# Optimization experiments

Hardware: AMD Instinct MI355X
Metric: run time of the kernel (lower is better)

Reference implementation:

```python
import jax, jax.numpy as jnp
import numpy as np

HEADS = 8
DIM_HEAD = 64
INNER = HEADS * DIM_HEAD  # 512
EPS = 1e-6


def layer_norm(x, gamma, beta):
    mu = jnp.mean(x, axis=-1, keepdims=True)
    var = jnp.var(x, axis=-1, keepdims=True)
    return (x - mu) * jax.lax.rsqrt(var + EPS) * gamma + beta


def setup_inputs() -> dict:
    key = jax.random.key(0)
    ks = jax.random.split(key, 8)
    b, n = 2, 2048
    s = lambda d: 1.0 / np.sqrt(d)
    return {
        "x": jax.random.normal(ks[0], (b, n, INNER), dtype=jnp.float32),
        # weights stored input-major: y = x @ W
        "w_qkv": jax.random.normal(ks[1], (INNER, 3 * INNER), dtype=jnp.float32) * s(INNER),
        "w_out": jax.random.normal(ks[2], (INNER, INNER), dtype=jnp.float32) * s(INNER),
        "b_out": jax.random.normal(ks[3], (INNER,), dtype=jnp.float32) * 0.01,
        "w_ff1": jax.random.normal(ks[4], (INNER, 4 * INNER), dtype=jnp.float32) * s(INNER),
        "w_ff2": jax.random.normal(ks[5], (4 * INNER, INNER), dtype=jnp.float32) * s(4 * INNER),
        "g1": jnp.ones((INNER,), dtype=jnp.float32),
        "be1": jnp.zeros((INNER,), dtype=jnp.float32),
        "g2": jnp.ones((INNER,), dtype=jnp.float32),
        "be2": jnp.zeros((INNER,), dtype=jnp.float32),
    }


def reference(x, w_qkv, w_out, b_out, w_ff1, w_ff2, g1, be1, g2, be2):
    b, n, _ = x.shape
    scale = DIM_HEAD ** (-0.5)
    qkv = x @ w_qkv  # [b, n, 3*inner]
    qkv = qkv.reshape(b, n, 3, HEADS, DIM_HEAD)
    q = qkv[:, :, 0].transpose(0, 2, 1, 3)  # [b, h, n, d]
    k = qkv[:, :, 1].transpose(0, 2, 1, 3)
    v = qkv[:, :, 2].transpose(0, 2, 1, 3)
    dots = jnp.einsum('bhqd,bhkd->bhqk', q, k) * scale
    attn = jax.nn.softmax(dots, axis=-1)
    out = jnp.einsum('bhqk,bhkd->bhqd', attn, v)
    out = out.transpose(0, 2, 1, 3).reshape(b, n, INNER)
    out = out @ w_out + b_out
    attn_res = layer_norm(x + out, g1, be1)
    # NOTE: no activation between the two FFN linears (faithful to source)
    ff = (attn_res @ w_ff1) @ w_ff2
    return layer_norm(attn_res + ff, g2, be2)
```

## Files before the change

### kernel.cpp

```cpp
#include <hip/hip_runtime.h>
#include <hip/hip_bf16.h>
#include <cstdint>
#include <cstddef>
#include <math.h>

#define HEADS 8
#define DHEAD 64
#define INNER 512
#define BATCH 2
#define SEQ   2048
#define MROWS (BATCH*SEQ)
#define LN_EPS 1e-6f
#define KSPLIT 2
#define KCHUNK (SEQ/KSPLIT)

typedef unsigned short u16;
typedef __attribute__((ext_vector_type(8))) short short8;
typedef __attribute__((ext_vector_type(4))) float f32x4;

#define MFMA16(a,b,c) __builtin_amdgcn_mfma_f32_16x16x32_bf16((a),(b),(c),0,0,0)

__device__ __forceinline__ u16 f2bf(float f) {
    __hip_bfloat16 h = __float2bfloat16(f);
    return *reinterpret_cast<u16*>(&h);
}
__device__ __forceinline__ void gl_lds16(const void* g, void* l) {
    __builtin_amdgcn_global_load_lds(
        (const __attribute__((address_space(1))) void*)g,
        (__attribute__((address_space(3))) void*)l, 16, 0, 0);
}

__global__ void f32_to_bf16_kernel(const float* __restrict__ in,
                                   u16* __restrict__ out, int n4) {
    int i = (blockIdx.x * 256 + threadIdx.x);
    if (i < n4) {
        float4 v = reinterpret_cast<const float4*>(in)[i];
        ushort4 o;
        o.x = f2bf(v.x); o.y = f2bf(v.y); o.z = f2bf(v.z); o.w = f2bf(v.w);
        reinterpret_cast<ushort4*>(out)[i] = o;
    }
}

__global__ void transpose_to_bf16_kernel(const float* __restrict__ B,
                                         u16* __restrict__ Bt, int K, int N) {
    __shared__ float T[32][33];
    const int tid = threadIdx.x;
    const int n0 = blockIdx.x * 32, k0 = blockIdx.y * 32;
    const int r = tid >> 3, c = (tid & 7) * 4;
    float4 v = *reinterpret_cast<const float4*>(&B[(size_t)(k0 + r) * N + n0 + c]);
    T[c + 0][r] = v.x; T[c + 1][r] = v.y; T[c + 2][r] = v.z; T[c + 3][r] = v.w;
    __syncthreads();
    ushort4 o;
    o.x = f2bf(T[r][c + 0]); o.y = f2bf(T[r][c + 1]);
    o.z = f2bf(T[r][c + 2]); o.w = f2bf(T[r][c + 3]);
    *reinterpret_cast<ushort4*>(&Bt[(size_t)(n0 + r) * K + k0 + c]) = o;
}

template<int BN, bool HAS_BIAS, bool OUT_F32, bool OUT_BF16>
__global__ __launch_bounds__(256) void gemm_bt(const u16* __restrict__ A,
                                               const u16* __restrict__ Bt,
                                               const float* __restrict__ bias,
                                               float* __restrict__ C,
                                               u16* __restrict__ Cb,
                                               int M, int N, int K) {
    constexpr int WN = BN / 2;
    constexpr int NT = WN / 16;
    __shared__ u16 As[128 * 32];
    __shared__ u16 Bs[BN * 32];
    const int tid = threadIdx.x;
    const int wave = tid >> 6, lane = tid & 63;
    const int l15 = lane & 15, quad = lane >> 4;
    const int wm = (wave >> 1) * 64, wn = (wave & 1) * WN;
    const int row0 = blockIdx.y * 128, col0 = blockIdx.x * BN;

    f32x4 acc[4][NT];
    #pragma unroll
    for (int mi = 0; mi < 4; ++mi)
        #pragma unroll
        for (int ni = 0; ni < NT; ++ni)
            #pragma unroll
            for (int e = 0; e < 4; ++e) acc[mi][ni][e] = 0.f;

    for (int k0 = 0; k0 < K; k0 += 32) {
        #pragma unroll
        for (int idx0 = 0; idx0 < 512 + BN * 4; idx0 += 256) {
            int idx = idx0 + tid;
            if (idx < 512) {
                int r = idx >> 2, ic = (idx & 3) * 8;
                gl_lds16(A + (size_t)(row0 + r) * K + k0 + ic, &As[idx * 8]);
            } else {
                int ib = idx - 512;
                int r = ib >> 2, ic = (ib & 3) * 8;
                gl_lds16(Bt + (size_t)(col0 + r) * K + k0 + ic, &Bs[ib * 8]);
            }
        }
        __syncthreads();

        short8 af[4], bf[NT];
        #pragma unroll
        for (int mi = 0; mi < 4; ++mi)
            af[mi] = *reinterpret_cast<const short8*>(&As[(wm + mi * 16 + l15) * 32 + quad * 8]);
        #pragma unroll
        for (int ni = 0; ni < NT; ++ni)
            bf[ni] = *reinterpret_cast<const short8*>(&Bs[(wn + ni * 16 + l15) * 32 + quad * 8]);
        #pragma unroll
        for (int mi = 0; mi < 4; ++mi)
            #pragma unroll
            for (int ni = 0; ni < NT; ++ni)
                acc[mi][ni] = MFMA16(af[mi], bf[ni], acc[mi][ni]);
        __syncthreads();
    }

    #pragma unroll
    for (int mi = 0; mi < 4; ++mi)
        #pragma unroll
        for (int ni = 0; ni < NT; ++ni)
            #pragma unroll
            for (int r = 0; r < 4; ++r) {
                int rr = row0 + wm + mi * 16 + quad * 4 + r;
                int cc = col0 + wn + ni * 16 + l15;
                float v = acc[mi][ni][r];
                if (HAS_BIAS) v += bias[cc];
                if (OUT_F32)  C[(size_t)rr * N + cc] = v;
                if (OUT_BF16) Cb[(size_t)rr * N + cc] = f2bf(v);
            }
}

__global__ __launch_bounds__(256) void attn_kernel(const u16* __restrict__ qkv,
                                                   float* __restrict__ Opart,
                                                   float* __restrict__ lpart) {
    __shared__ u16 QP[64][72];
    __shared__ u16 Ks[64][72];
    __shared__ u16 VT[64][72];

    const int tid = threadIdx.x;
    const int wave = tid >> 6, lane = tid & 63;
    const int l15 = lane & 15, quad = lane >> 4;
    const int qt = blockIdx.x, bh = blockIdx.y, ks = blockIdx.z;
    const int b = bh >> 3, h = bh & 7;
    const int w16 = wave * 16;

    const u16* qbase = qkv + (size_t)(b * SEQ + qt * 64) * 1536 + h * 64;

    #pragma unroll
    for (int j = 0; j < 2; ++j) {
        int c = tid + j * 256;
        int r = c >> 3, ch = c & 7;
        *reinterpret_cast<uint4*>(&QP[r][ch * 8]) =
            *reinterpret_cast<const uint4*>(qbase + (size_t)r * 1536 + ch * 8);
    }
    __syncthreads();

    short8 qf[2];
    #pragma unroll
    for (int ksk = 0; ksk < 2; ++ksk)
        qf[ksk] = *reinterpret_cast<const short8*>(&QP[w16 + l15][ksk * 32 + quad * 8]);

    f32x4 oacc[4];
    float lsum[4];
    #pragma unroll
    for (int di = 0; di < 4; ++di)
        #pragma unroll
        for (int e = 0; e < 4; ++e) oacc[di][e] = 0.f;
    #pragma unroll
    for (int r = 0; r < 4; ++r) lsum[r] = 0.f;

    const float scale = 0.125f;

    for (int kt = 0; kt < KCHUNK / 64; ++kt) {
        const u16* kvbase = qkv +
            (size_t)(b * SEQ + ks * KCHUNK + kt * 64) * 1536 + h * 64;
        #pragma unroll
        for (int j = 0; j < 2; ++j) {
            int c = tid + j * 256;
            int r = c >> 3, ch = c & 7;
            *reinterpret_cast<uint4*>(&Ks[r][ch * 8]) =
                *reinterpret_cast<const uint4*>(kvbase + 512 + (size_t)r * 1536 + ch * 8);
        }
        {
            int kj = tid & 63, d0 = (tid >> 6) * 16;
            const u16* vp = kvbase + 1024 + (size_t)kj * 1536 + d0;
            u16 tmp[16];
            *reinterpret_cast<uint4*>(tmp)     = *reinterpret_cast<const uint4*>(vp);
            *reinterpret_cast<uint4*>(tmp + 8) = *reinterpret_cast<const uint4*>(vp + 8);
            #pragma unroll
            for (int i = 0; i < 16; ++i) VT[d0 + i][kj] = tmp[i];
        }
        __syncthreads();

        f32x4 sacc[4];
        #pragma unroll
        for (int ni = 0; ni < 4; ++ni)
            #pragma unroll
            for (int e = 0; e < 4; ++e) sacc[ni][e] = 0.f;
        #pragma unroll
        for (int ksk = 0; ksk < 2; ++ksk) {
            short8 kf[4];
            #pragma unroll
            for (int ni = 0; ni < 4; ++ni)
                kf[ni] = *reinterpret_cast<const short8*>(
                    &Ks[ni * 16 + l15][ksk * 32 + quad * 8]);
            #pragma unroll
            for (int ni = 0; ni < 4; ++ni)
                sacc[ni] = MFMA16(qf[ksk], kf[ni], sacc[ni]);
        }

        #pragma unroll
        for (int ni = 0; ni < 4; ++ni)
            #pragma unroll
            for (int r = 0; r < 4; ++r) {
                float p = __expf(sacc[ni][r] * scale);
                lsum[r] += p;
                QP[w16 + quad * 4 + r][ni * 16 + l15] = f2bf(p);
            }

        #pragma unroll
        for (int ksk = 0; ksk < 2; ++ksk) {
            short8 pf = *reinterpret_cast<const short8*>(
                &QP[w16 + l15][ksk * 32 + quad * 8]);
            #pragma unroll
            for (int di = 0; di < 4; ++di) {
                short8 vf = *reinterpret_cast<const short8*>(
                    &VT[di * 16 + l15][ksk * 32 + quad * 8]);
                oacc[di] = MFMA16(pf, vf, oacc[di]);
            }
        }
        __syncthreads();
    }

    #pragma unroll
    for (int r = 0; r < 4; ++r) {
        float v = lsum[r];
        v += __shfl_xor(v, 1); v += __shfl_xor(v, 2);
        v += __shfl_xor(v, 4); v += __shfl_xor(v, 8);
        lsum[r] = v;
    }

    const size_t pbase = ((size_t)(ks * 16 + bh) * SEQ + qt * 64);
    #pragma unroll
    for (int di = 0; di < 4; ++di)
        #pragma unroll
        for (int r = 0; r < 4; ++r)
            Opart[(pbase + w16 + quad * 4 + r) * 64 + di * 16 + l15] = oacc[di][r];
    if (l15 == 0)
        #pragma unroll
        for (int r = 0; r < 4; ++r)
            lpart[pbase + w16 + quad * 4 + r] = lsum[r];
}

__global__ void attn_combine_kernel(const float* __restrict__ Opart,
                                    const float* __restrict__ lpart,
                                    u16* __restrict__ attn_b) {
    int i = blockIdx.x * 256 + threadIdx.x;
    int e = i * 4;
    int row = e >> 9;
    int c = e & 511;
    int h = c >> 6, d = c & 63;
    int b = row >> 11, srow = row & 2047;
    int bh = b * 8 + h;

    size_t i0 = ((size_t)bh * SEQ + srow) * 64 + d;
    size_t i1 = ((size_t)(16 + bh) * SEQ + srow) * 64 + d;
    float4 o0 = *reinterpret_cast<const float4*>(&Opart[i0]);
    float4 o1 = *reinterpret_cast<const float4*>(&Opart[i1]);
    float l = lpart[(size_t)bh * SEQ + srow] + lpart[(size_t)(16 + bh) * SEQ + srow];
    float li = 1.f / l;
    ushort4 o;
    o.x = f2bf((o0.x + o1.x) * li);
    o.y = f2bf((o0.y + o1.y) * li);
    o.z = f2bf((o0.z + o1.z) * li);
    o.w = f2bf((o0.w + o1.w) * li);
    *reinterpret_cast<ushort4*>(&attn_b[(size_t)row * INNER + c]) = o;
}

__global__ void ln_kernel(const float* __restrict__ a,
                          const float* __restrict__ bsrc,
                          const float* __restrict__ g,
                          const float* __restrict__ be,
                          float* __restrict__ out32,
                          u16* __restrict__ out16) {
    __shared__ float red[256];
    const int row = blockIdx.x, tid = threadIdx.x;
    const size_t off = (size_t)row * INNER;
    const int c0 = tid, c1 = tid + 256;

    float v0 = a[off + c0] + bsrc[off + c0];
    float v1 = a[off + c1] + bsrc[off + c1];

    red[tid] = v0 + v1;
    __syncthreads();
    for (int s = 128; s > 0; s >>= 1) {
        if (tid < s) red[tid] += red[tid + s];
        __syncthreads();
    }
    float mu = red[0] * (1.f / INNER);
    __syncthreads();

    float d0 = v0 - mu, d1 = v1 - mu;
    red[tid] = d0 * d0 + d1 * d1;
    __syncthreads();
    for (int s = 128; s > 0; s >>= 1) {
        if (tid < s) red[tid] += red[tid + s];
        __syncthreads();
    }
    float rstd = rsqrtf(red[0] * (1.f / INNER) + LN_EPS);

    float y0 = d0 * rstd * g[c0] + be[c0];
    float y1 = d1 * rstd * g[c1] + be[c1];
    if (out32) { out32[off + c0] = y0; out32[off + c1] = y1; }
    if (out16) { out16[off + c0] = f2bf(y0); out16[off + c1] = f2bf(y1); }
}

extern "C" void kernel_launch(void* const* d_in, const int* in_sizes, int n_in,
                              void* d_out, int out_size, void* d_ws, size_t ws_size,
                              hipStream_t stream) {
    const float* x     = (const float*)d_in[0];
    const float* w_qkv = (const float*)d_in[1];
    const float* w_out = (const float*)d_in[2];
    const float* b_out = (const float*)d_in[3];
    const float* w_ff1 = (const float*)d_in[4];
    const float* w_ff2 = (const float*)d_in[5];
    const float* g1    = (const float*)d_in[6];
    const float* be1   = (const float*)d_in[7];
    const float* g2    = (const float*)d_in[8];
    const float* be2   = (const float*)d_in[9];
    float* out = (float*)d_out;

    char* W = (char*)d_ws;
    u16*   w_outT     = (u16*)  (W + 0);
    u16*   w_ff1T     = (u16*)  (W + 524288);
    u16*   w_ff2T     = (u16*)  (W + 2621440);
    u16*   qkv_b      = (u16*)  (W + 4718592);
    float* proj       = (float*)(W + 4718592);
    float* ff2        = (float*)(W + 4718592);
    u16*   attn_res_b = (u16*)  (W + 13107200);
    u16*   x_b        = (u16*)  (W + 17301504);
    u16*   w_qkvT     = (u16*)  (W + 21495808);
    float* Opart      = (float*)(W + 17301504);
    u16*   ff1_b      = (u16*)  (W + 17301504);
    float* lpart      = (float*)(W + 34078720);
    u16*   attn_b     = (u16*)  (W + 34340864);
    float* attn_res   = (float*)(W + 38535168);

    f32_to_bf16_kernel<<<(MROWS * INNER / 4 + 255) / 256, 256, 0, stream>>>(
        x, x_b, MROWS * INNER / 4);
    transpose_to_bf16_kernel<<<dim3(1536 / 32, 512 / 32),  256, 0, stream>>>(w_qkv, w_qkvT, 512, 1536);
    transpose_to_bf16_kernel<<<dim3(512 / 32,  512 / 32),  256, 0, stream>>>(w_out, w_outT, 512, 512);
    transpose_to_bf16_kernel<<<dim3(2048 / 32, 512 / 32),  256, 0, stream>>>(w_ff1, w_ff1T, 512, 2048);
    transpose_to_bf16_kernel<<<dim3(512 / 32,  2048 / 32), 256, 0, stream>>>(w_ff2, w_ff2T, 2048, 512);

    gemm_bt<128, false, false, true><<<dim3(1536 / 128, MROWS / 128), 256, 0, stream>>>(
        x_b, w_qkvT, nullptr, nullptr, qkv_b, MROWS, 1536, INNER);

    attn_kernel<<<dim3(SEQ / 64, BATCH * HEADS, KSPLIT), 256, 0, stream>>>(
        qkv_b, Opart, lpart);

    attn_combine_kernel<<<(MROWS * INNER / 4) / 256, 256, 0, stream>>>(
        Opart, lpart, attn_b);

    gemm_bt<64, true, true, false><<<dim3(INNER / 64, MROWS / 128), 256, 0, stream>>>(
        attn_b, w_outT, b_out, proj, nullptr, MROWS, INNER, INNER);

    ln_kernel<<<MROWS, 256, 0, stream>>>(x, proj, g1, be1, attn_res, attn_res_b);

    gemm_bt<128, false, false, true><<<dim3(2048 / 128, MROWS / 128), 256, 0, stream>>>(
        attn_res_b, w_ff1T, nullptr, nullptr, ff1_b, MROWS, 2048, INNER);

    gemm_bt<64, false, true, false><<<dim3(INNER / 64, MROWS / 128), 256, 0, stream>>>(
        ff1_b, w_ff2T, nullptr, ff2, nullptr, MROWS, INNER, 2048);

    ln_kernel<<<MROWS, 256, 0, stream>>>(attn_res, ff2, g2, be2, out, nullptr);
}
```

Measured before the change: 242.2 us.

## Write Q/K and transposed V from QKV GEMM, prefetch attention tiles, split-K FF2

```diff
diff --git a/kernel.cpp b/kernel.cpp
--- a/kernel.cpp
+++ b/kernel.cpp
@@ -20,6 +20,9 @@
 
 #define MFMA16(a,b,c) __builtin_amdgcn_mfma_f32_16x16x32_bf16((a),(b),(c),0,0,0)
 
+__device__ __forceinline__ float bf2f(u16 u) {
+    union { float f; uint32_t i; } x; x.i = ((uint32_t)u) << 16; return x.f;
+}
 __device__ __forceinline__ u16 f2bf(float f) {
     __hip_bfloat16 h = __float2bfloat16(f);
     return *reinterpret_cast<u16*>(&h);
@@ -56,12 +59,13 @@
     *reinterpret_cast<ushort4*>(&Bt[(size_t)(n0 + r) * K + k0 + c]) = o;
 }
 
-template<int BN, bool HAS_BIAS, bool OUT_F32, bool OUT_BF16>
+template<int BN, int EPI>
 __global__ __launch_bounds__(256) void gemm_bt(const u16* __restrict__ A,
                                                const u16* __restrict__ Bt,
                                                const float* __restrict__ bias,
                                                float* __restrict__ C,
                                                u16* __restrict__ Cb,
+                                               u16* __restrict__ Vt,
                                                int M, int N, int K) {
     constexpr int WN = BN / 2;
     constexpr int NT = WN / 16;
@@ -73,6 +77,12 @@
     const int wm = (wave >> 1) * 64, wn = (wave & 1) * WN;
     const int row0 = blockIdx.y * 128, col0 = blockIdx.x * BN;
 
+    int kbase = 0, kend = K;
+    if (EPI == 3) {
+        int chunk = K / gridDim.z;
+        kbase = blockIdx.z * chunk; kend = kbase + chunk;
+    }
+
     f32x4 acc[4][NT];
     #pragma unroll
     for (int mi = 0; mi < 4; ++mi)
@@ -81,7 +91,7 @@
             #pragma unroll
             for (int e = 0; e < 4; ++e) acc[mi][ni][e] = 0.f;
 
-    for (int k0 = 0; k0 < K; k0 += 32) {
+    for (int k0 = kbase; k0 < kend; k0 += 32) {
         #pragma unroll
         for (int idx0 = 0; idx0 < 512 + BN * 4; idx0 += 256) {
             int idx = idx0 + tid;
@@ -114,19 +124,44 @@
     #pragma unroll
     for (int mi = 0; mi < 4; ++mi)
         #pragma unroll
-        for (int ni = 0; ni < NT; ++ni)
-            #pragma unroll
-            for (int r = 0; r < 4; ++r) {
-                int rr = row0 + wm + mi * 16 + quad * 4 + r;
-                int cc = col0 + wn + ni * 16 + l15;
-                float v = acc[mi][ni][r];
-                if (HAS_BIAS) v += bias[cc];
-                if (OUT_F32)  C[(size_t)rr * N + cc] = v;
-                if (OUT_BF16) Cb[(size_t)rr * N + cc] = f2bf(v);
+        for (int ni = 0; ni < NT; ++ni) {
+            const int cc = col0 + wn + ni * 16 + l15;
+            const int rr0 = row0 + wm + mi * 16 + quad * 4;
+            if (EPI == 0) {
+                #pragma unroll
+                for (int r = 0; r < 4; ++r)
+                    Cb[(size_t)(rr0 + r) * N + cc] = f2bf(acc[mi][ni][r]);
+            } else if (EPI == 1) {
+                #pragma unroll
+                for (int r = 0; r < 4; ++r)
+                    C[(size_t)(rr0 + r) * N + cc] = acc[mi][ni][r] + bias[cc];
+            } else if (EPI == 3) {
+                float* Cz = C + (size_t)blockIdx.z * M * N;
+                #pragma unroll
+                for (int r = 0; r < 4; ++r)
+                    Cz[(size_t)(rr0 + r) * N + cc] = acc[mi][ni][r];
+            } else {
+                if (cc < 1024) {
+                    size_t base = (cc < 512) ? (size_t)cc
+                                             : ((size_t)MROWS * 512 + cc - 512);
+                    #pragma unroll
+                    for (int r = 0; r < 4; ++r)
+                        Cb[base + (size_t)(rr0 + r) * 512] = f2bf(acc[mi][ni][r]);
+                } else {
+                    int hh = (cc - 1024) >> 6, dd = (cc - 1024) & 63;
+                    int bb = rr0 >> 11, srow = rr0 & 2047;
+                    ushort4 o;
+                    o.x = f2bf(acc[mi][ni][0]); o.y = f2bf(acc[mi][ni][1]);
+                    o.z = f2bf(acc[mi][ni][2]); o.w = f2bf(acc[mi][ni][3]);
+                    *reinterpret_cast<ushort4*>(
+                        &Vt[(((size_t)(bb * 8 + hh) * 64 + dd) << 11) + srow]) = o;
+                }
             }
-}
-
-__global__ __launch_bounds__(256) void attn_kernel(const u16* __restrict__ qkv,
+        }
+}
+
+__global__ __launch_bounds__(256) void attn_kernel(const u16* __restrict__ qk_b,
+                                                   const u16* __restrict__ vT_b,
                                                    float* __restrict__ Opart,
                                                    float* __restrict__ lpart) {
     __shared__ u16 QP[64][72];
@@ -139,22 +174,21 @@
     const int qt = blockIdx.x, bh = blockIdx.y, ks = blockIdx.z;
     const int b = bh >> 3, h = bh & 7;
     const int w16 = wave * 16;
-
-    const u16* qbase = qkv + (size_t)(b * SEQ + qt * 64) * 1536 + h * 64;
-
-    #pragma unroll
-    for (int j = 0; j < 2; ++j) {
-        int c = tid + j * 256;
-        int r = c >> 3, ch = c & 7;
-        *reinterpret_cast<uint4*>(&QP[r][ch * 8]) =
-            *reinterpret_cast<const uint4*>(qbase + (size_t)r * 1536 + ch * 8);
+    const int r0 = tid >> 3, r1 = r0 + 32;
+    const int ch = (tid & 7) * 8;
+
+    {
+        const u16* qb = qk_b + (size_t)(b * SEQ + qt * 64) * 512 + h * 64;
+        *reinterpret_cast<uint4*>(&QP[r0][ch]) =
+            *reinterpret_cast<const uint4*>(&qb[(size_t)r0 * 512 + ch]);
+        *reinterpret_cast<uint4*>(&QP[r1][ch]) =
+            *reinterpret_cast<const uint4*>(&qb[(size_t)r1 * 512 + ch]);
     }
     __syncthreads();
 
     short8 qf[2];
-    #pragma unroll
-    for (int ksk = 0; ksk < 2; ++ksk)
-        qf[ksk] = *reinterpret_cast<const short8*>(&QP[w16 + l15][ksk * 32 + quad * 8]);
+    qf[0] = *reinterpret_cast<const short8*>(&QP[w16 + l15][quad * 8]);
+    qf[1] = *reinterpret_cast<const short8*>(&QP[w16 + l15][32 + quad * 8]);
 
     f32x4 oacc[4];
     float lsum[4];
@@ -165,28 +199,32 @@
     #pragma unroll
     for (int r = 0; r < 4; ++r) lsum[r] = 0.f;
 
-    const float scale = 0.125f;
+    const u16* kb = qk_b + (size_t)MROWS * 512
+                  + (size_t)(b * SEQ + ks * KCHUNK) * 512 + h * 64;
+    const u16* vb = vT_b + (size_t)bh * 64 * 2048 + ks * KCHUNK;
+
+    uint4 kr0 = *reinterpret_cast<const uint4*>(&kb[(size_t)r0 * 512 + ch]);
+    uint4 kr1 = *reinterpret_cast<const uint4*>(&kb[(size_t)r1 * 512 + ch]);
+    uint4 vr0 = *reinterpret_cast<const uint4*>(&vb[(size_t)r0 * 2048 + ch]);
+    uint4 vr1 = *reinterpret_cast<const uint4*>(&vb[(size_t)r1 * 2048 + ch]);
+
+    const float CEXP = 0.18033688011110918f;
 
     for (int kt = 0; kt < KCHUNK / 64; ++kt) {
-        const u16* kvbase = qkv +
-            (size_t)(b * SEQ + ks * KCHUNK + kt * 64) * 1536 + h * 64;
-        #pragma unroll
-        for (int j = 0; j < 2; ++j) {
-            int c = tid + j * 256;
-            int r = c >> 3, ch = c & 7;
-            *reinterpret_cast<uint4*>(&Ks[r][ch * 8]) =
-                *reinterpret_cast<const uint4*>(kvbase + 512 + (size_t)r * 1536 + ch * 8);
+        *reinterpret_cast<uint4*>(&Ks[r0][ch]) = kr0;
+        *reinterpret_cast<uint4*>(&Ks[r1][ch]) = kr1;
+        *reinterpret_cast<uint4*>(&VT[r0][ch]) = vr0;
+        *reinterpret_cast<uint4*>(&VT[r1][ch]) = vr1;
+        __syncthreads();
+
+        if (kt + 1 < KCHUNK / 64) {
+            const u16* kb2 = kb + (size_t)(kt + 1) * 64 * 512;
+            const u16* vb2 = vb + (kt + 1) * 64;
+            kr0 = *reinterpret_cast<const uint4*>(&kb2[(size_t)r0 * 512 + ch]);
+            kr1 = *reinterpret_cast<const uint4*>(&kb2[(size_t)r1 * 512 + ch]);
+            vr0 = *reinterpret_cast<const uint4*>(&vb2[(size_t)r0 * 2048 + ch]);
+            vr1 = *reinterpret_cast<const uint4*>(&vb2[(size_t)r1 * 2048 + ch]);
         }
-        {
-            int kj = tid & 63, d0 = (tid >> 6) * 16;
-            const u16* vp = kvbase + 1024 + (size_t)kj * 1536 + d0;
-            u16 tmp[16];
-            *reinterpret_cast<uint4*>(tmp)     = *reinterpret_cast<const uint4*>(vp);
-            *reinterpret_cast<uint4*>(tmp + 8) = *reinterpret_cast<const uint4*>(vp + 8);
-            #pragma unroll
-            for (int i = 0; i < 16; ++i) VT[d0 + i][kj] = tmp[i];
-        }
-        __syncthreads();
 
         f32x4 sacc[4];
         #pragma unroll
@@ -209,7 +247,7 @@
         for (int ni = 0; ni < 4; ++ni)
             #pragma unroll
             for (int r = 0; r < 4; ++r) {
-                float p = __expf(sacc[ni][r] * scale);
+                float p = exp2f(sacc[ni][r] * CEXP);
                 lsum[r] += p;
                 QP[w16 + quad * 4 + r][ni * 16 + l15] = f2bf(p);
             }
@@ -273,8 +311,10 @@
     *reinterpret_cast<ushort4*>(&attn_b[(size_t)row * INNER + c]) = o;
 }
 
-__global__ void ln_kernel(const float* __restrict__ a,
-                          const float* __restrict__ bsrc,
+template<bool A16, bool TWO>
+__global__ void ln_kernel(const void* __restrict__ a_,
+                          const float* __restrict__ s0,
+                          const float* __restrict__ s1,
                           const float* __restrict__ g,
                           const float* __restrict__ be,
                           float* __restrict__ out32,
@@ -284,8 +324,17 @@
     const size_t off = (size_t)row * INNER;
     const int c0 = tid, c1 = tid + 256;
 
-    float v0 = a[off + c0] + bsrc[off + c0];
-    float v1 = a[off + c1] + bsrc[off + c1];
+    float a0, a1;
+    if (A16) {
+        const u16* a = (const u16*)a_;
+        a0 = bf2f(a[off + c0]); a1 = bf2f(a[off + c1]);
+    } else {
+        const float* a = (const float*)a_;
+        a0 = a[off + c0]; a1 = a[off + c1];
+    }
+    float v0 = a0 + s0[off + c0];
+    float v1 = a1 + s0[off + c1];
+    if (TWO) { v0 += s1[off + c0]; v1 += s1[off + c1]; }
 
     red[tid] = v0 + v1;
     __syncthreads();
@@ -330,17 +379,17 @@
     u16*   w_outT     = (u16*)  (W + 0);
     u16*   w_ff1T     = (u16*)  (W + 524288);
     u16*   w_ff2T     = (u16*)  (W + 2621440);
-    u16*   qkv_b      = (u16*)  (W + 4718592);
-    float* proj       = (float*)(W + 4718592);
-    float* ff2        = (float*)(W + 4718592);
-    u16*   attn_res_b = (u16*)  (W + 13107200);
+    u16*   qk_b       = (u16*)  (W + 4718592);
+    u16*   attn_b     = (u16*)  (W + 4718592);
+    u16*   attn_res_b = (u16*)  (W + 4718592);
+    float* proj       = (float*)(W + 8912896);
+    u16*   ff1_b      = (u16*)  (W + 8912896);
+    u16*   vT_b       = (u16*)  (W + 13107200);
     u16*   x_b        = (u16*)  (W + 17301504);
     u16*   w_qkvT     = (u16*)  (W + 21495808);
     float* Opart      = (float*)(W + 17301504);
-    u16*   ff1_b      = (u16*)  (W + 17301504);
     float* lpart      = (float*)(W + 34078720);
-    u16*   attn_b     = (u16*)  (W + 34340864);
-    float* attn_res   = (float*)(W + 38535168);
+    float* ff2p       = (float*)(W + 25690112);
 
     f32_to_bf16_kernel<<<(MROWS * INNER / 4 + 255) / 256, 256, 0, stream>>>(
         x, x_b, MROWS * INNER / 4);
@@ -349,25 +398,27 @@
     transpose_to_bf16_kernel<<<dim3(2048 / 32, 512 / 32),  256, 0, stream>>>(w_ff1, w_ff1T, 512, 2048);
     transpose_to_bf16_kernel<<<dim3(512 / 32,  2048 / 32), 256, 0, stream>>>(w_ff2, w_ff2T, 2048, 512);
 
-    gemm_bt<128, false, false, true><<<dim3(1536 / 128, MROWS / 128), 256, 0, stream>>>(
-        x_b, w_qkvT, nullptr, nullptr, qkv_b, MROWS, 1536, INNER);
+    gemm_bt<128, 2><<<dim3(1536 / 128, MROWS / 128), 256, 0, stream>>>(
+        x_b, w_qkvT, nullptr, nullptr, qk_b, vT_b, MROWS, 1536, INNER);
 
     attn_kernel<<<dim3(SEQ / 64, BATCH * HEADS, KSPLIT), 256, 0, stream>>>(
-        qkv_b, Opart, lpart);
+        qk_b, vT_b, Opart, lpart);
 
     attn_combine_kernel<<<(MROWS * INNER / 4) / 256, 256, 0, stream>>>(
         Opart, lpart, attn_b);
 
-    gemm_bt<64, true, true, false><<<dim3(INNER / 64, MROWS / 128), 256, 0, stream>>>(
-        attn_b, w_outT, b_out, proj, nullptr, MROWS, INNER, INNER);
-
-    ln_kernel<<<MROWS, 256, 0, stream>>>(x, proj, g1, be1, attn_res, attn_res_b);
-
-    gemm_bt<128, false, false, true><<<dim3(2048 / 128, MROWS / 128), 256, 0, stream>>>(
-        attn_res_b, w_ff1T, nullptr, nullptr, ff1_b, MROWS, 2048, INNER);
-
-    gemm_bt<64, false, true, false><<<dim3(INNER / 64, MROWS / 128), 256, 0, stream>>>(
-        ff1_b, w_ff2T, nullptr, ff2, nullptr, MROWS, INNER, 2048);
-
-    ln_kernel<<<MROWS, 256, 0, stream>>>(attn_res, ff2, g2, be2, out, nullptr);
-}
+    gemm_bt<64, 1><<<dim3(INNER / 64, MROWS / 128), 256, 0, stream>>>(
+        attn_b, w_outT, b_out, proj, nullptr, nullptr, MROWS, INNER, INNER);
+
+    ln_kernel<false, false><<<MROWS, 256, 0, stream>>>(
+        x, proj, nullptr, g1, be1, nullptr, attn_res_b);
+
+    gemm_bt<128, 0><<<dim3(2048 / 128, MROWS / 128), 256, 0, stream>>>(
+        attn_res_b, w_ff1T, nullptr, nullptr, ff1_b, nullptr, MROWS, 2048, INNER);
+
+    gemm_bt<64, 3><<<dim3(INNER / 64, MROWS / 128, 2), 256, 0, stream>>>(
+        ff1_b, w_ff2T, nullptr, ff2p, nullptr, nullptr, MROWS, INNER, 2048);
+
+    ln_kernel<true, true><<<MROWS, 256, 0, stream>>>(
+        attn_res_b, ff2p, ff2p + (size_t)MROWS * INNER, g2, be2, out, nullptr);
+}
```

After: 236.0 us. -2.6%, faster.
